# Kernel optimization log

Measured on AMD Instinct MI355X. Metric: run time of the kernel, lower is better.

Reference implementation:

```python
import jax, jax.numpy as jnp
import numpy as np

N = 100_000            # nodes
E = 1_600_000          # edges per metapath
IN = 256               # input features
HEADS, DIM = 8, 16     # heads * dim = hidden_channels
HIDDEN = HEADS * DIM   # 128
OUT = 4                # classes
NEG_SLOPE = 0.2


def setup_inputs() -> dict:
    key = jax.random.key(0)
    ks = jax.random.split(key, 16)
    s = 1.0 / np.sqrt(HIDDEN)
    return {
        "x": jax.random.normal(ks[0], (N, IN), jnp.float32),
        "edge_index0": jax.random.randint(ks[1], (2, E), 0, N, jnp.int64),
        "edge_index1": jax.random.randint(ks[2], (2, E), 0, N, jnp.int64),
        "proj_w": jax.random.normal(ks[3], (IN, HIDDEN), jnp.float32) / np.sqrt(IN),
        "proj_b": jnp.zeros((HIDDEN,), jnp.float32),
        "att_src0": jax.random.normal(ks[4], (HEADS, DIM), jnp.float32) * s,
        "att_dst0": jax.random.normal(ks[5], (HEADS, DIM), jnp.float32) * s,
        "att_src1": jax.random.normal(ks[6], (HEADS, DIM), jnp.float32) * s,
        "att_dst1": jax.random.normal(ks[7], (HEADS, DIM), jnp.float32) * s,
        "k_lin_w": jax.random.normal(ks[8], (HIDDEN, HIDDEN), jnp.float32) * s,
        "k_lin_b": jnp.zeros((HIDDEN,), jnp.float32),
        "q": jax.random.normal(ks[9], (HIDDEN,), jnp.float32) * s,
        "lin_w": jax.random.normal(ks[10], (HIDDEN, OUT), jnp.float32) * s,
        "lin_b": jnp.zeros((OUT,), jnp.float32),
    }


def _metapath_conv(xp, a_src, a_dst, src, dst):
    # xp: [N,H,D]; a_src, a_dst: [H,D]; src/dst: [E]
    alpha_src = (xp * a_src).sum(-1)                     # [N,H]
    alpha_dst = (xp * a_dst).sum(-1)                     # [N,H]
    e = jax.nn.leaky_relu(alpha_src[src] + alpha_dst[dst], NEG_SLOPE)  # [E,H]
    emax = jax.ops.segment_max(e, dst, num_segments=N)  # [N,H] (stable softmax)
    e = jnp.exp(e - emax[dst])
    denom = jax.ops.segment_sum(e, dst, num_segments=N)
    alpha = e / (denom[dst] + 1e-16)                     # edge softmax per dst
    msg = xp[src] * alpha[..., None]                     # [E,H,D]
    out = jax.ops.segment_sum(msg, dst, num_segments=N)  # [N,H,D]
    return jax.nn.relu(out.reshape(N, HIDDEN))


def reference(x, edge_index0, edge_index1, proj_w, proj_b,
              att_src0, att_dst0, att_src1, att_dst1,
              k_lin_w, k_lin_b, q, lin_w, lin_b):
    # shared node-type projection
    xp = (x @ proj_w + proj_b).reshape(N, HEADS, DIM)
    # per-metapath GAT-style convolutions (dropout=0.6 is eval no-op)
    outs = jnp.stack([
        _metapath_conv(xp, att_src0, att_dst0, edge_index0[0], edge_index0[1]),
        _metapath_conv(xp, att_src1, att_dst1, edge_index1[0], edge_index1[1]),
    ])                                                    # [M,N,HIDDEN]
    # semantic attention over metapaths
    k = jnp.tanh(outs @ k_lin_w + k_lin_b).mean(axis=1)  # [M,HIDDEN]
    attn = jax.nn.softmax((k * q).sum(-1))               # [M]
    fused = (attn[:, None, None] * outs).sum(0)          # [N,HIDDEN]
    return fused @ lin_w + lin_b                          # [N,OUT]
```

## Files before the change

kernel.cpp:

```cpp
#include <hip/hip_runtime.h>
#include <hip/hip_bf16.h>

#define NN 100000
#define EE 1600000
#define HID 128
#define NEG 0.2f
#define CAP 64
#define BSH 9
#define NB 196
#define CAPB 9216
#define EBLK 4096

typedef __attribute__((ext_vector_type(8))) short short8;
typedef __attribute__((ext_vector_type(4))) float f32x4;

static __device__ __forceinline__ float bf2f(short s) {
  union { float f; unsigned u; } c;
  c.u = ((unsigned)(unsigned short)s) << 16;
  return c.f;
}

static __device__ __forceinline__ float exp2_fast(float x) {
  float r;
  asm("v_exp_f32 %0, %1" : "=v"(r) : "v"(x));
  return r;
}

static __device__ __forceinline__ float tanh_fast(float x) {
  float a = fminf(fmaxf(x * 2.885390082f, -40.f), 40.f);
  float e = exp2_fast(a);
  float r = __builtin_amdgcn_rcpf(e + 1.f);
  return fmaf(-2.f, r, 1.f);
}

__global__ __launch_bounds__(256) void k_wprep(const float* __restrict__ w,
    const float* __restrict__ kw, short* __restrict__ wTg, short* __restrict__ kwTg) {
  int i = blockIdx.x * 256 + threadIdx.x;
  if (i < 32768) {
    int n = i >> 8, k = i & 255;
    __hip_bfloat16 b = __float2bfloat16(w[k * 128 + n]);
    wTg[i] = *(short*)&b;
  } else if (i < 49152) {
    int j = i - 32768;
    int n = j >> 7, k = j & 127;
    __hip_bfloat16 b = __float2bfloat16(kw[k * 128 + n]);
    kwTg[j] = *(short*)&b;
  }
}

#define PWS 264
#define PNT ((NN + 15) / 16)
#define PGX 512

__global__ __launch_bounds__(256) void k_proj(const float* __restrict__ x,
    const short* __restrict__ wTg, const float* __restrict__ bias,
    const float* __restrict__ a0s, const float* __restrict__ a0d,
    const float* __restrict__ a1s, const float* __restrict__ a1d,
    __hip_bfloat16* __restrict__ xph,
    float* __restrict__ as0, float* __restrict__ ad0,
    float* __restrict__ as1, float* __restrict__ ad1) {
  __shared__ short wT[128 * PWS];
  const int tid = threadIdx.x;
  for (int i = tid; i < 4096; i += 256) {
    int n = i >> 5, kc = i & 31;
    *(short8*)&wT[n * PWS + kc * 8] = *(const short8*)&wTg[n * 256 + kc * 8];
  }
  const int lane = tid & 63, wave = tid >> 6;
  const int rowgrp = lane >> 4, lcol = lane & 15;
  const bool b3 = (lcol & 8) != 0, b2 = (lcol & 4) != 0;
  const int ttype = (lcol >> 2) & 3;
  float* __restrict__ ap = (ttype == 0) ? as0 : (ttype == 1) ? ad0
                         : (ttype == 2) ? as1 : ad1;
  float bv[8], AS0[8], AD0[8], AS1[8], AD1[8];
  const float L2E = 1.44269504f;
#pragma unroll
  for (int ct = 0; ct < 8; ct++) {
    bv[ct] = bias[ct * 16 + lcol];
    AS0[ct] = a0s[ct * 16 + lcol] * L2E;
    AD0[ct] = a0d[ct * 16 + lcol] * L2E;
    AS1[ct] = a1s[ct * 16 + lcol] * L2E;
    AD1[ct] = a1d[ct * 16 + lcol] * L2E;
  }
  __syncthreads();
  for (int tile = blockIdx.x * 4 + wave; tile < PNT; tile += gridDim.x * 4) {
    const int r0 = tile * 16;
    int row = r0 + lcol;
    if (row >= NN) row = NN - 1;
    const float* xr = x + (size_t)row * 256 + rowgrp * 8;
    short8 af[8];
#pragma unroll
    for (int kc = 0; kc < 8; kc++) {
      float4 u0 = *(const float4*)(xr + kc * 32);
      float4 u1 = *(const float4*)(xr + kc * 32 + 4);
      union { short8 v; __hip_bfloat162 h[4]; } u;
      u.h[0] = __float22bfloat162_rn(make_float2(u0.x, u0.y));
      u.h[1] = __float22bfloat162_rn(make_float2(u0.z, u0.w));
      u.h[2] = __float22bfloat162_rn(make_float2(u1.x, u1.y));
      u.h[3] = __float22bfloat162_rn(make_float2(u1.z, u1.w));
      af[kc] = u.v;
    }
#pragma unroll
    for (int ct = 0; ct < 8; ct++) {
      f32x4 acc = {0.f, 0.f, 0.f, 0.f};
#pragma unroll
      for (int kc = 0; kc < 8; kc++) {
        short8 bf = *(const short8*)&wT[(ct * 16 + lcol) * PWS + kc * 32 + rowgrp * 8];
        acc = __builtin_amdgcn_mfma_f32_16x16x32_bf16(af[kc], bf, acc, 0, 0, 0);
      }
#pragma unroll
      for (int r = 0; r < 4; r++) {
        int orow = r0 + rowgrp * 4 + r;
        float xv = acc[r] + bv[ct];
        if (orow < NN) {
          __hip_bfloat16 ob = __float2bfloat16(xv);
          ((short*)xph)[(size_t)orow * 128 + ct * 16 + lcol] = *(short*)&ob;
        }
        float q0 = xv * AS0[ct], q1 = xv * AD0[ct], q2 = xv * AS1[ct], q3 = xv * AD1[ct];
        float va = (b3 ? q2 : q0) + __shfl_xor(b3 ? q0 : q2, 8, 64);
        float vb = (b3 ? q3 : q1) + __shfl_xor(b3 ? q1 : q3, 8, 64);
        float v  = (b2 ? vb : va) + __shfl_xor(b2 ? va : vb, 4, 64);
        v += __shfl_xor(v, 2, 64);
        v += __shfl_xor(v, 1, 64);
        if ((lcol & 3) == 0 && orow < NN) ap[orow * 8 + ct] = v;
      }
    }
  }
}

__global__ __launch_bounds__(256) void k_bin(const int* __restrict__ ei0,
    const int* __restrict__ ei1, int* __restrict__ gcur, int* __restrict__ binned) {
  const int p = blockIdx.y;
  const int* __restrict__ ei = p ? ei1 : ei0;
  const int* __restrict__ src = ei;
  const int* __restrict__ dst = ei + EE;
  int* __restrict__ gc = gcur + p * 256;
  int* __restrict__ bn = binned + (size_t)p * NB * CAPB;
  __shared__ int cntL[NB], baseL[NB], posL[NB];
  const int t = threadIdx.x;
  const int e0 = blockIdx.x * EBLK;
  const int e1 = min(e0 + EBLK, EE);
  for (int i = t; i < NB; i += 256) { cntL[i] = 0; posL[i] = 0; }
  __syncthreads();
  for (int e = e0 + t; e < e1; e += 256)
    atomicAdd(&cntL[dst[e] >> BSH], 1);
  __syncthreads();
  for (int i = t; i < NB; i += 256)
    baseL[i] = atomicAdd(&gc[i], cntL[i]);
  __syncthreads();
  for (int e = e0 + t; e < e1; e += 256) {
    int d = dst[e];
    int b = d >> BSH;
    int off = baseL[b] + atomicAdd(&posL[b], 1);
    if (off < CAPB) bn[b * CAPB + off] = (src[e] << BSH) | (d & 511);
  }
}

__global__ __launch_bounds__(512) void k_build(const int* __restrict__ gcur,
    const int* __restrict__ binned, int* __restrict__ cnt, int* __restrict__ csr) {
  const int p = blockIdx.y, b = blockIdx.x, t = threadIdx.x;
  const int* __restrict__ bn = binned + (size_t)p * NB * CAPB + (size_t)b * CAPB;
  const int n = min(gcur[p * 256 + b], CAPB);
  int* __restrict__ cs = csr + (size_t)p * NN * CAP;
  __shared__ int lc[512];
  lc[t] = 0;
  __syncthreads();
  const int node0 = b << BSH;
  for (int i = t; i < n; i += 512) {
    int v = bn[i];
    int ln = v & 511;
    int off = atomicAdd(&lc[ln], 1);
    if (off < CAP) cs[(size_t)(node0 + ln) * CAP + off] = v >> BSH;
  }
  __syncthreads();
  int n0 = node0 + t;
  if (n0 < NN) cnt[p * NN + n0] = lc[t];
}


#define EDGE_BODY(sv)                                      \
  {                                                        \
    unsigned s = (unsigned)(sv);                           \
    float t = asrc[s * 8u + h];                            \
    __hip_bfloat162 v = xph[s * 64u + lane];               \
    float tt = t + ad;                                     \
    float al = exp2_fast(fmaxf(tt, NEG * tt));             \
    denom += al;                                           \
    float2 f = __bfloat1622float2(v);                      \
    a0 = fmaf(al, f.x, a0);                                \
    a1 = fmaf(al, f.y, a1);                                \
  }

__global__ __launch_bounds__(256) void k_aggr(const __hip_bfloat162* __restrict__ xph,
    const float* __restrict__ as0, const float* __restrict__ ad0,
    const float* __restrict__ as1, const float* __restrict__ ad1,
    const int* __restrict__ cnt, const int* __restrict__ csr,
    __hip_bfloat162* __restrict__ h0, __hip_bfloat162* __restrict__ h1) {
  const int p = blockIdx.y;
  const unsigned lane = threadIdx.x & 63;
  int node = blockIdx.x * 4 + (threadIdx.x >> 6);
  if (node >= NN) return;
  node = __builtin_amdgcn_readfirstlane(node);
  const float* __restrict__ asrc = p ? as1 : as0;
  const float* __restrict__ adst = p ? ad1 : ad0;
  const int* __restrict__ cs = csr + ((size_t)p * NN + node) * CAP;
  __hip_bfloat162* __restrict__ hout = p ? h1 : h0;
  const unsigned h = lane >> 3;
  const float ad = adst[(unsigned)node * 8u + h];
  const int deg = min(cnt[p * NN + node], CAP);

  float denom = 1e-16f, a0 = 0.f, a1 = 0.f;
  int e = 0;
  for (; e + 8 <= deg; e += 8) {
    int4 q0 = *(const int4*)&cs[e];
    int4 q1 = *(const int4*)&cs[e + 4];
    EDGE_BODY(q0.x) EDGE_BODY(q0.y) EDGE_BODY(q0.z) EDGE_BODY(q0.w)
    EDGE_BODY(q1.x) EDGE_BODY(q1.y) EDGE_BODY(q1.z) EDGE_BODY(q1.w)
  }
  for (; e + 4 <= deg; e += 4) {
    int4 q0 = *(const int4*)&cs[e];
    EDGE_BODY(q0.x) EDGE_BODY(q0.y) EDGE_BODY(q0.z) EDGE_BODY(q0.w)
  }
  for (; e < deg; e++) EDGE_BODY(cs[e])
  float inv = 1.f / denom;
  hout[(size_t)node * 64 + lane] =
      __float22bfloat162_rn(make_float2(fmaxf(a0 * inv, 0.f), fmaxf(a1 * inv, 0.f)));
}

#define KWS 136
#define NTILES ((NN + 63) / 64)
#define SEMGX 512

__global__ __launch_bounds__(256) void k_sem(const __hip_bfloat16* __restrict__ h0,
    const __hip_bfloat16* __restrict__ h1, const short* __restrict__ kwTg,
    const float* __restrict__ kb, const float* __restrict__ lw,
    float* __restrict__ ksum, float* __restrict__ o0, float* __restrict__ o1) {
  __shared__ short kwT[128 * KWS];
  __shared__ float red[4][128];
  __shared__ float lwS[512];
  const int tid = threadIdx.x;
  const int m = blockIdx.y;
  const short* __restrict__ hc = (const short*)(m ? h1 : h0);
  float* __restrict__ oc = m ? o1 : o0;
  for (int i = tid; i < 2048; i += 256) {
    int n = i >> 4, kc = i & 15;
    *(short8*)&kwT[n * KWS + kc * 8] = *(const short8*)&kwTg[n * 128 + kc * 8];
  }
  for (int l = tid; l < 512; l += 256) lwS[l] = lw[l];
  const int lane = tid & 63;
  const int wave = tid >> 6;
  const int rowgrp = lane >> 4;
  const int lcol = lane & 15;
  float partial[8] = {};
  float kbv[8];
#pragma unroll
  for (int ct = 0; ct < 8; ct++) kbv[ct] = kb[ct * 16 + lcol];
  __syncthreads();
  for (int tile = blockIdx.x; tile < NTILES; tile += SEMGX) {
    int n0 = tile * 64 + wave * 16;
    int row = n0 + lcol;
    if (row >= NN) row = 0;
    const short* hr = hc + (size_t)row * 128 + rowgrp * 8;
    short8 afrag[4];
#pragma unroll
    for (int kc = 0; kc < 4; kc++) afrag[kc] = *(const short8*)(hr + kc * 32);
    float op[4] = {0.f, 0.f, 0.f, 0.f};
#pragma unroll
    for (int kc = 0; kc < 4; kc++) {
      union { short8 v; short s[8]; } u;
      u.v = afrag[kc];
#pragma unroll
      for (int j = 0; j < 8; j++) {
        float hv = bf2f(u.s[j]);
        const float4 lv = *(const float4*)&lwS[(kc * 32 + rowgrp * 8 + j) * 4];
        op[0] = fmaf(hv, lv.x, op[0]);
        op[1] = fmaf(hv, lv.y, op[1]);
        op[2] = fmaf(hv, lv.z, op[2]);
        op[3] = fmaf(hv, lv.w, op[3]);
      }
    }
#pragma unroll
    for (int c = 0; c < 4; c++) {
      op[c] += __shfl_xor(op[c], 16, 64);
      op[c] += __shfl_xor(op[c], 32, 64);
    }
    int orow = n0 + lcol;
    if (rowgrp == 0 && orow < NN) {
      float4 ov = make_float4(op[0], op[1], op[2], op[3]);
      *(float4*)&oc[(size_t)orow * 4] = ov;
    }
#pragma unroll
    for (int ct = 0; ct < 8; ct++) {
      f32x4 acc = {0.f, 0.f, 0.f, 0.f};
#pragma unroll
      for (int kc = 0; kc < 4; kc++) {
        short8 bfrag = *(const short8*)&kwT[(ct * 16 + lcol) * KWS + kc * 32 + rowgrp * 8];
        acc = __builtin_amdgcn_mfma_f32_16x16x32_bf16(afrag[kc], bfrag, acc, 0, 0, 0);
      }
#pragma unroll
      for (int r = 0; r < 4; r++) {
        int node = n0 + rowgrp * 4 + r;
        if (node < NN) partial[ct] += tanh_fast(acc[r] + kbv[ct]);
      }
    }
  }
#pragma unroll
  for (int ct = 0; ct < 8; ct++) {
    partial[ct] += __shfl_xor(partial[ct], 16, 64);
    partial[ct] += __shfl_xor(partial[ct], 32, 64);
  }
  if (lane < 16) {
#pragma unroll
    for (int ct = 0; ct < 8; ct++) red[wave][ct * 16 + lane] = partial[ct];
  }
  __syncthreads();
  if (tid < 128) {
    float s = red[0][tid] + red[1][tid] + red[2][tid] + red[3][tid];
    atomicAdd(&ksum[m * 128 + tid], s);
  }
}

__global__ __launch_bounds__(256) void k_blend(const float* __restrict__ o0,
    const float* __restrict__ o1, const float* __restrict__ lb,
    const float* __restrict__ ksum, const float* __restrict__ q,
    float* __restrict__ out) {
  __shared__ float aw[2];
  const int t = threadIdx.x;
  if (t < 64) {
    float qa = q[t], qb = q[t + 64];
    float s0 = fmaf(ksum[t], qa, ksum[t + 64] * qb);
    float s1 = fmaf(ksum[128 + t], qa, ksum[192 + t] * qb);
#pragma unroll
    for (int off = 1; off < 64; off <<= 1) {
      s0 += __shfl_xor(s0, off, 64);
      s1 += __shfl_xor(s1, off, 64);
    }
    if (t == 0) {
      float l0 = s0 * (1.f / NN), l1 = s1 * (1.f / NN);
      float mx = fmaxf(l0, l1);
      float e0 = __expf(l0 - mx), e1 = __expf(l1 - mx);
      float inv = 1.f / (e0 + e1);
      aw[0] = e0 * inv;
      aw[1] = e1 * inv;
    }
  }
  __syncthreads();
  int i = blockIdx.x * 256 + t;
  if (i < NN * 4)
    out[i] = aw[0] * o0[i] + aw[1] * o1[i] + lb[i & 3];
}

extern "C" void kernel_launch(void* const* d_in, const int* in_sizes, int n_in,
                              void* d_out, int out_size, void* d_ws, size_t ws_size,
                              hipStream_t stream) {
  const float* x      = (const float*)d_in[0];
  const int*   ei0    = (const int*)d_in[1];
  const int*   ei1    = (const int*)d_in[2];
  const float* proj_w = (const float*)d_in[3];
  const float* proj_b = (const float*)d_in[4];
  const float* a0s    = (const float*)d_in[5];
  const float* a0d    = (const float*)d_in[6];
  const float* a1s    = (const float*)d_in[7];
  const float* a1d    = (const float*)d_in[8];
  const float* klw    = (const float*)d_in[9];
  const float* klb    = (const float*)d_in[10];
  const float* q      = (const float*)d_in[11];
  const float* lw     = (const float*)d_in[12];
  const float* lb     = (const float*)d_in[13];
  float* out = (float*)d_out;

  char* ws = (char*)d_ws;
  size_t off = 0;
  auto alloc = [&](size_t bytes) -> void* {
    size_t o = (off + 255) & ~(size_t)255;
    off = o + bytes;
    return (void*)(ws + o);
  };
  __hip_bfloat162* xph = (__hip_bfloat162*)alloc((size_t)NN * 128 * 2);
  __hip_bfloat162* h0  = (__hip_bfloat162*)alloc((size_t)NN * 128 * 2);
  __hip_bfloat162* h1  = (__hip_bfloat162*)alloc((size_t)NN * 128 * 2);
  float* as0  = (float*)alloc((size_t)NN * 8 * 4);
  float* ad0  = (float*)alloc((size_t)NN * 8 * 4);
  float* as1  = (float*)alloc((size_t)NN * 8 * 4);
  float* ad1  = (float*)alloc((size_t)NN * 8 * 4);
  int* cnt    = (int*)alloc((size_t)2 * NN * 4);
  float* ksum = (float*)alloc(256 * 4);
  int* gcur   = (int*)alloc(2 * 256 * 4);
  int* csr    = (int*)alloc((size_t)2 * NN * CAP * 4);
  int* binned = (int*)alloc((size_t)2 * NB * CAPB * 4);
  short* wTg  = (short*)alloc(32768 * 2);
  short* kwTg = (short*)alloc(16384 * 2);
  float* o0   = (float*)alloc((size_t)NN * 4 * 4);
  float* o1   = (float*)alloc((size_t)NN * 4 * 4);

  hipMemsetAsync(cnt, 0, (size_t)2 * NN * 4 + 256 * 4 + 2 * 256 * 4, stream);

  k_wprep<<<dim3(192), 256, 0, stream>>>(proj_w, klw, wTg, kwTg);
  k_proj<<<dim3(PGX), 256, 0, stream>>>(x, wTg, proj_b, a0s, a0d, a1s, a1d,
                                        (__hip_bfloat16*)xph, as0, ad0, as1, ad1);
  k_bin<<<dim3((EE + EBLK - 1) / EBLK, 2), 256, 0, stream>>>(ei0, ei1, gcur, binned);
  k_build<<<dim3(NB, 2), 512, 0, stream>>>(gcur, binned, cnt, csr);
  k_aggr<<<dim3((NN + 3) / 4, 2), 256, 0, stream>>>(xph, as0, ad0, as1, ad1,
                                                    cnt, csr, h0, h1);
  k_sem<<<dim3(SEMGX, 2), 256, 0, stream>>>((const __hip_bfloat16*)h0,
                                            (const __hip_bfloat16*)h1, kwTg, klb, lw,
                                            ksum, o0, o1);
  k_blend<<<dim3((NN * 4 + 255) / 256), 256, 0, stream>>>(o0, o1, lb, ksum, q, out);
}
```

Before: 527.1 us.

## Merge bin/weight-prep and build/projection kernels to overlap independent stages

Fuses edge binning with weight transpose into one launch, and CSR build with the projection GEMM into another, so independent work runs concurrently on different blocks. The binning pass now reads each dst once, holding edge values and local offsets in registers instead of making a second pass with shared atomics. The memset shrinks because cnt is now written fully by the build blocks. Block-role branching raises register and LDS pressure in the merged kernels, and projection now uses 512-thread blocks.

```diff
diff --git a/kernel.cpp b/kernel.cpp
--- a/kernel.cpp
+++ b/kernel.cpp
@@ -10,6 +10,9 @@
 #define NB 196
 #define CAPB 9216
 #define EBLK 4096
+#define NBINB 391
+#define NBUILD 392
+#define NPROJ 512
 
 typedef __attribute__((ext_vector_type(8))) short short8;
 typedef __attribute__((ext_vector_type(4))) float f32x4;
@@ -33,35 +36,102 @@
   return fmaf(-2.f, r, 1.f);
 }
 
-__global__ __launch_bounds__(256) void k_wprep(const float* __restrict__ w,
-    const float* __restrict__ kw, short* __restrict__ wTg, short* __restrict__ kwTg) {
-  int i = blockIdx.x * 256 + threadIdx.x;
-  if (i < 32768) {
-    int n = i >> 8, k = i & 255;
-    __hip_bfloat16 b = __float2bfloat16(w[k * 128 + n]);
-    wTg[i] = *(short*)&b;
-  } else if (i < 49152) {
-    int j = i - 32768;
-    int n = j >> 7, k = j & 127;
-    __hip_bfloat16 b = __float2bfloat16(kw[k * 128 + n]);
-    kwTg[j] = *(short*)&b;
+__global__ __launch_bounds__(256) void k_prep(const int* __restrict__ ei0,
+    const int* __restrict__ ei1, const float* __restrict__ w,
+    const float* __restrict__ kw, int* __restrict__ gcur,
+    int* __restrict__ binned, short* __restrict__ wTg, short* __restrict__ kwTg) {
+  const int bid = blockIdx.x;
+  const int t = threadIdx.x;
+  if (bid >= 2 * NBINB) {
+    int i = (bid - 2 * NBINB) * 256 + t;
+    if (i < 32768) {
+      int n = i >> 8, k = i & 255;
+      __hip_bfloat16 b = __float2bfloat16(w[k * 128 + n]);
+      wTg[i] = *(short*)&b;
+    } else if (i < 49152) {
+      int j = i - 32768;
+      int n = j >> 7, k = j & 127;
+      __hip_bfloat16 b = __float2bfloat16(kw[k * 128 + n]);
+      kwTg[j] = *(short*)&b;
+    }
+    return;
+  }
+  const int p = bid >= NBINB;
+  const int bx = p ? bid - NBINB : bid;
+  const int* __restrict__ ei = p ? ei1 : ei0;
+  const int* __restrict__ src = ei;
+  const int* __restrict__ dst = ei + EE;
+  int* __restrict__ gc = gcur + p * 256;
+  int* __restrict__ bn = binned + (size_t)p * NB * CAPB;
+  __shared__ int cntL[NB], baseL[NB];
+  const int e0 = bx * EBLK;
+  const int e1 = min(e0 + EBLK, EE);
+  for (int i = t; i < NB; i += 256) cntL[i] = 0;
+  __syncthreads();
+  int vj[16], bj[16];
+#pragma unroll
+  for (int j = 0; j < 16; j++) {
+    int e = e0 + t + j * 256;
+    bj[j] = -1;
+    if (e < e1) {
+      int d = dst[e];
+      int b = d >> BSH;
+      int off = atomicAdd(&cntL[b], 1);
+      vj[j] = (src[e] << BSH) | (d & 511);
+      bj[j] = (b << 14) | off;
+    }
+  }
+  __syncthreads();
+  for (int i = t; i < NB; i += 256) baseL[i] = atomicAdd(&gc[i], cntL[i]);
+  __syncthreads();
+#pragma unroll
+  for (int j = 0; j < 16; j++) {
+    if (bj[j] >= 0) {
+      int b = bj[j] >> 14;
+      int off = baseL[b] + (bj[j] & 16383);
+      if (off < CAPB) bn[b * CAPB + off] = vj[j];
+    }
   }
 }
 
 #define PWS 264
 #define PNT ((NN + 15) / 16)
-#define PGX 512
-
-__global__ __launch_bounds__(256) void k_proj(const float* __restrict__ x,
-    const short* __restrict__ wTg, const float* __restrict__ bias,
+
+__global__ __launch_bounds__(512) void k_mid(
+    const int* __restrict__ gcur, const int* __restrict__ binned,
+    int* __restrict__ cnt, int* __restrict__ csr,
+    const float* __restrict__ x, const short* __restrict__ wTg,
+    const float* __restrict__ bias,
     const float* __restrict__ a0s, const float* __restrict__ a0d,
     const float* __restrict__ a1s, const float* __restrict__ a1d,
     __hip_bfloat16* __restrict__ xph,
     float* __restrict__ as0, float* __restrict__ ad0,
     float* __restrict__ as1, float* __restrict__ ad1) {
   __shared__ short wT[128 * PWS];
+  const int bid = blockIdx.x;
   const int tid = threadIdx.x;
-  for (int i = tid; i < 4096; i += 256) {
+  if (bid < NBUILD) {
+    int* lc = (int*)wT;
+    const int p = bid >= 196, b = p ? bid - 196 : bid;
+    const int* __restrict__ bn = binned + (size_t)p * NB * CAPB + (size_t)b * CAPB;
+    const int n = min(gcur[p * 256 + b], CAPB);
+    int* __restrict__ cs = csr + (size_t)p * NN * CAP;
+    lc[tid] = 0;
+    __syncthreads();
+    const int node0 = b << BSH;
+    for (int i = tid; i < n; i += 512) {
+      int v = bn[i];
+      int ln = v & 511;
+      int off = atomicAdd(&lc[ln], 1);
+      if (off < CAP) cs[(size_t)(node0 + ln) * CAP + off] = v >> BSH;
+    }
+    __syncthreads();
+    int n0 = node0 + tid;
+    if (n0 < NN) cnt[p * NN + n0] = lc[tid];
+    return;
+  }
+  const int pb = bid - NBUILD;
+  for (int i = tid; i < 4096; i += 512) {
     int n = i >> 5, kc = i & 31;
     *(short8*)&wT[n * PWS + kc * 8] = *(const short8*)&wTg[n * 256 + kc * 8];
   }
@@ -82,7 +152,7 @@
     AD1[ct] = a1d[ct * 16 + lcol] * L2E;
   }
   __syncthreads();
-  for (int tile = blockIdx.x * 4 + wave; tile < PNT; tile += gridDim.x * 4) {
+  for (int tile = pb * 8 + wave; tile < PNT; tile += NPROJ * 8) {
     const int r0 = tile * 16;
     int row = r0 + lcol;
     if (row >= NN) row = NN - 1;
@@ -125,55 +195,6 @@
       }
     }
   }
-}
-
-__global__ __launch_bounds__(256) void k_bin(const int* __restrict__ ei0,
-    const int* __restrict__ ei1, int* __restrict__ gcur, int* __restrict__ binned) {
-  const int p = blockIdx.y;
-  const int* __restrict__ ei = p ? ei1 : ei0;
-  const int* __restrict__ src = ei;
-  const int* __restrict__ dst = ei + EE;
-  int* __restrict__ gc = gcur + p * 256;
-  int* __restrict__ bn = binned + (size_t)p * NB * CAPB;
-  __shared__ int cntL[NB], baseL[NB], posL[NB];
-  const int t = threadIdx.x;
-  const int e0 = blockIdx.x * EBLK;
-  const int e1 = min(e0 + EBLK, EE);
-  for (int i = t; i < NB; i += 256) { cntL[i] = 0; posL[i] = 0; }
-  __syncthreads();
-  for (int e = e0 + t; e < e1; e += 256)
-    atomicAdd(&cntL[dst[e] >> BSH], 1);
-  __syncthreads();
-  for (int i = t; i < NB; i += 256)
-    baseL[i] = atomicAdd(&gc[i], cntL[i]);
-  __syncthreads();
-  for (int e = e0 + t; e < e1; e += 256) {
-    int d = dst[e];
-    int b = d >> BSH;
-    int off = baseL[b] + atomicAdd(&posL[b], 1);
-    if (off < CAPB) bn[b * CAPB + off] = (src[e] << BSH) | (d & 511);
-  }
-}
-
-__global__ __launch_bounds__(512) void k_build(const int* __restrict__ gcur,
-    const int* __restrict__ binned, int* __restrict__ cnt, int* __restrict__ csr) {
-  const int p = blockIdx.y, b = blockIdx.x, t = threadIdx.x;
-  const int* __restrict__ bn = binned + (size_t)p * NB * CAPB + (size_t)b * CAPB;
-  const int n = min(gcur[p * 256 + b], CAPB);
-  int* __restrict__ cs = csr + (size_t)p * NN * CAP;
-  __shared__ int lc[512];
-  lc[t] = 0;
-  __syncthreads();
-  const int node0 = b << BSH;
-  for (int i = t; i < n; i += 512) {
-    int v = bn[i];
-    int ln = v & 511;
-    int off = atomicAdd(&lc[ln], 1);
-    if (off < CAP) cs[(size_t)(node0 + ln) * CAP + off] = v >> BSH;
-  }
-  __syncthreads();
-  int n0 = node0 + t;
-  if (n0 < NN) cnt[p * NN + n0] = lc[t];
 }
 
 
@@ -382,9 +403,9 @@
   float* ad0  = (float*)alloc((size_t)NN * 8 * 4);
   float* as1  = (float*)alloc((size_t)NN * 8 * 4);
   float* ad1  = (float*)alloc((size_t)NN * 8 * 4);
-  int* cnt    = (int*)alloc((size_t)2 * NN * 4);
   float* ksum = (float*)alloc(256 * 4);
   int* gcur   = (int*)alloc(2 * 256 * 4);
+  int* cnt    = (int*)alloc((size_t)2 * NN * 4);
   int* csr    = (int*)alloc((size_t)2 * NN * CAP * 4);
   int* binned = (int*)alloc((size_t)2 * NB * CAPB * 4);
   short* wTg  = (short*)alloc(32768 * 2);
@@ -392,13 +413,15 @@
   float* o0   = (float*)alloc((size_t)NN * 4 * 4);
   float* o1   = (float*)alloc((size_t)NN * 4 * 4);
 
-  hipMemsetAsync(cnt, 0, (size_t)2 * NN * 4 + 256 * 4 + 2 * 256 * 4, stream);
-
-  k_wprep<<<dim3(192), 256, 0, stream>>>(proj_w, klw, wTg, kwTg);
-  k_proj<<<dim3(PGX), 256, 0, stream>>>(x, wTg, proj_b, a0s, a0d, a1s, a1d,
-                                        (__hip_bfloat16*)xph, as0, ad0, as1, ad1);
-  k_bin<<<dim3((EE + EBLK - 1) / EBLK, 2), 256, 0, stream>>>(ei0, ei1, gcur, binned);
-  k_build<<<dim3(NB, 2), 512, 0, stream>>>(gcur, binned, cnt, csr);
+  hipMemsetAsync(ksum, 0, 256 * 4 + 2 * 256 * 4, stream);
+
+  k_prep<<<dim3(2 * NBINB + 192), 256, 0, stream>>>(ei0, ei1, proj_w, klw,
+                                                    gcur, binned, wTg, kwTg);
+  k_mid<<<dim3(NBUILD + NPROJ), 512, 0, stream>>>(gcur, binned, cnt, csr,
+                                                  x, wTg, proj_b,
+                                                  a0s, a0d, a1s, a1d,
+                                                  (__hip_bfloat16*)xph,
+                                                  as0, ad0, as1, ad1);
   k_aggr<<<dim3((NN + 3) / 4, 2), 256, 0, stream>>>(xph, as0, ad0, as1, ad1,
                                                     cnt, csr, h0, h1);
   k_sem<<<dim3(SEMGX, 2), 256, 0, stream>>>((const __hip_bfloat16*)h0,
```

After: 531.3 us. No clear change (+0.8%).
